# Performance work log

Hardware: AMD Instinct MI355X
Metric: run time of the kernel (lower is better)

## Reference

```python
import jax, jax.numpy as jnp
import numpy as np

HEAD_DIM = 128      # pooled entry dim (nope 64 + rope 64)
ROPE_DIM = 64       # trailing rotary slice
RATIO = 32          # compress_rate_csa: window stride; window width = 2*RATIO
ROPE_THETA = 10000.0
NEG = -1e9          # finite stand-in for -inf gate fill (softmax weight ~ 0)


def rotate_half_interleaved(x):
    # matches HF convention used with cos.repeat_interleave(2): pairs (x0,x1) -> (-x1,x0)
    x1 = x[..., 0::2]
    x2 = x[..., 1::2]
    return jnp.stack([-x2, x1], axis=-1).reshape(x.shape)


def setup_inputs() -> dict:
    key = jax.random.key(0)
    k1, k2, k3, k4 = jax.random.split(key, 4)
    B, S, H = 4, 8192, 4096
    return {
        "hidden_states": jax.random.normal(k1, (B, S, H), dtype=jnp.float32),
        "w_kv": jax.random.normal(k2, (H, 2 * HEAD_DIM), dtype=jnp.float32) * 0.02,
        "w_gate": jax.random.normal(k3, (H, 2 * HEAD_DIM), dtype=jnp.float32) * 0.02,
        "position_bias": jax.random.normal(k4, (2 * RATIO, HEAD_DIM), dtype=jnp.float32) * 0.02,
    }


def reference(hidden_states, w_kv, w_gate, position_bias):
    B, S, H = hidden_states.shape
    d, r = HEAD_DIM, RATIO
    n = S // r  # number of overlapping windows (stride r, width 2r)

    # projections C = H @ W^KV, Z = H @ W^Z   -> [B, S, 2d]
    kv = hidden_states @ w_kv
    gate = hidden_states @ w_gate

    chunk_kv = kv[:, : n * r].reshape(B, n, r, 2 * d)
    chunk_gate = gate[:, : n * r].reshape(B, n, r, 2 * d)

    # _overlap_pool: stitch each window's low-channel slice onto the prior
    # window's high-channel slice; window 0 prior half = 0 (kv) / -inf (gate).
    kv_lo, kv_hi = chunk_kv[..., :d], chunk_kv[..., d:]
    g_lo, g_hi = chunk_gate[..., :d], chunk_gate[..., d:]
    prev_kv = jnp.concatenate([jnp.zeros_like(kv_lo[:, :1]), kv_lo[:, :-1]], axis=1)
    prev_g = jnp.concatenate([jnp.full_like(g_lo[:, :1], NEG), g_lo[:, :-1]], axis=1)
    win_kv = jnp.concatenate([prev_kv, kv_hi], axis=2)   # [B, n, 2r, d]
    win_g = jnp.concatenate([prev_g, g_hi], axis=2)      # [B, n, 2r, d]

    # softmax-gated pooling over window tokens (per channel), with position bias
    w = jax.nn.softmax(win_g + position_bias[None, None], axis=2)
    pooled = jnp.sum(w * win_kv, axis=2)                 # [B, n, d]

    # RoPE on trailing rope slice at deterministic absolute window positions
    positions = jnp.arange(n, dtype=jnp.float32) * r     # first_pool_position = 0
    inv_freq = 1.0 / (ROPE_THETA ** (jnp.arange(0, ROPE_DIM, 2, dtype=jnp.float32) / ROPE_DIM))
    freqs = positions[:, None] * inv_freq[None, :]       # [n, ROPE_DIM/2]
    cos = jnp.repeat(jnp.cos(freqs), 2, axis=-1)         # [n, ROPE_DIM]
    sin = jnp.repeat(jnp.sin(freqs), 2, axis=-1)

    nope, rope = pooled[..., :-ROPE_DIM], pooled[..., -ROPE_DIM:]
    rotated = rope * cos[None] + rotate_half_interleaved(rope) * sin[None]
    return jnp.concatenate([nope, rotated], axis=-1)     # [B, n, d]
```

## Files before the change

### kernel.cpp

```cpp
#include <hip/hip_runtime.h>
#include <hip/hip_bf16.h>
#include <math.h>

typedef unsigned short ushort_t;
typedef __bf16 bf16x8 __attribute__((ext_vector_type(8)));
typedef float floatx4 __attribute__((ext_vector_type(4)));
typedef float floatx8 __attribute__((ext_vector_type(8)));

#define NEG_BIG -1000000000.0f

__device__ __forceinline__ float b2f(ushort_t u) {
  union { unsigned int i; float f; } v;
  v.i = ((unsigned int)u) << 16;
  return v.f;
}
__device__ __forceinline__ ushort_t f2b(float f) {
  union { float f; unsigned int i; } v;
  v.f = f;
  unsigned int r = v.i + 0x7fffu + ((v.i >> 16) & 1u);
  return (ushort_t)(r >> 16);
}

__device__ __forceinline__ float loadC(const float* p) { return *p; }
__device__ __forceinline__ float loadC(const ushort_t* p) { return b2f(*p); }
__device__ __forceinline__ void storeC(float* p, float v) { *p = v; }
__device__ __forceinline__ void storeC(ushort_t* p, float v) { *p = f2b(v); }

__global__ __launch_bounds__(256) void transpose_w_kernel(
    const float* __restrict__ w_kv, const float* __restrict__ w_gate,
    ushort_t* __restrict__ Wt) {
  __shared__ float tile[64][65];
  const int K0 = blockIdx.x * 64;
  const int N0c = blockIdx.y * 64;
  const float* src = (N0c < 256) ? w_kv : w_gate;
  const int N0 = N0c & 255;
  const int t = threadIdx.x;
#pragma unroll
  for (int i = 0; i < 16; ++i) {
    int l = t + 256 * i;
    int r = l >> 6, c = l & 63;
    tile[r][c] = src[(size_t)(K0 + r) * 256 + N0 + c];
  }
  __syncthreads();
#pragma unroll
  for (int i = 0; i < 16; ++i) {
    int l = t + 256 * i;
    int r = l >> 6, c = l & 63;
    Wt[(size_t)(N0c + r) * 4096 + K0 + c] = f2b(tile[c][r]);
  }
}

template <typename CT>
__global__ __launch_bounds__(256, 2) void gemm_kernel(
    const float* __restrict__ A,
    const ushort_t* __restrict__ Bt,
    CT* __restrict__ C) {
  constexpr int K = 4096;
  __shared__ __align__(16) ushort_t As[128 * 64];
  __shared__ __align__(16) ushort_t Bs[128 * 64];

  const int mt = blockIdx.x >> 2;
  const int nt = blockIdx.x & 3;
  const int m0 = mt * 128, n0 = nt * 128;
  const int tid = threadIdx.x;
  const int w = tid >> 6, lane = tid & 63;
  const int wm = w >> 1, wn = w & 1;
  const int sr = lane >> 3;
  const int sc = (lane & 7) * 8;
  const int ar = tid >> 3;
  const int ac = (tid & 7) * 8;
  const int q = lane >> 4, sid = lane & 15;

  floatx4 acc[4][4];
#pragma unroll
  for (int i = 0; i < 4; ++i)
#pragma unroll
    for (int j = 0; j < 4; ++j) acc[i][j] = (floatx4)0.0f;

  for (int kt = 0; kt < K; kt += 64) {
    __syncthreads();
#pragma unroll
    for (int i = 0; i < 4; ++i) {
      const int chunk = i * 4 + w;
      const int row = chunk * 8 + sr;
      const ushort_t* g = Bt + (size_t)(n0 + row) * K + kt + sc;
      __builtin_amdgcn_global_load_lds(
          (const __attribute__((address_space(1))) void*)g,
          (__attribute__((address_space(3))) void*)(Bs + chunk * 512), 16, 0, 0);
    }
#pragma unroll
    for (int p = 0; p < 4; ++p) {
      const int row = p * 32 + ar;
      const float* g = A + (size_t)(m0 + row) * K + kt + ac;
      floatx8 f = *(const floatx8*)g;
      bf16x8 h = __builtin_convertvector(f, bf16x8);
      *(bf16x8*)(As + row * 64 + ac) = h;
    }
    __syncthreads();

#pragma unroll
    for (int ks = 0; ks < 64; ks += 32) {
      bf16x8 af[4], bfr[4];
#pragma unroll
      for (int i = 0; i < 4; ++i)
        af[i] = *(const bf16x8*)(As + (wm * 64 + i * 16 + sid) * 64 + ks + q * 8);
#pragma unroll
      for (int j = 0; j < 4; ++j)
        bfr[j] = *(const bf16x8*)(Bs + (wn * 64 + j * 16 + sid) * 64 + ks + q * 8);
#pragma unroll
      for (int i = 0; i < 4; ++i)
#pragma unroll
        for (int j = 0; j < 4; ++j)
          acc[i][j] = __builtin_amdgcn_mfma_f32_16x16x32_bf16(af[i], bfr[j],
                                                              acc[i][j], 0, 0, 0);
    }
  }

#pragma unroll
  for (int i = 0; i < 4; ++i) {
#pragma unroll
    for (int j = 0; j < 4; ++j) {
#pragma unroll
      for (int r = 0; r < 4; ++r) {
        const int row = m0 + wm * 64 + i * 16 + q * 4 + r;
        const int col = n0 + wn * 64 + j * 16 + sid;
        storeC(&C[(size_t)row * 512 + col], acc[i][j][r]);
      }
    }
  }
}

template <typename CT>
__global__ __launch_bounds__(128) void pool_rope_kernel(
    const CT* __restrict__ C,
    const float* __restrict__ pb,
    float* __restrict__ out) {
  const int blk = blockIdx.x;
  const int j = blk & 255;
  const int d = threadIdx.x;

  const size_t base_hi = (size_t)blk * 32 * 512;
  const size_t base_lo = base_hi - (size_t)32 * 512;

  float m = -INFINITY, l = 0.f, o = 0.f;
#pragma unroll 8
  for (int t = 0; t < 64; ++t) {
    float g, kv;
    const float bias = pb[t * 128 + d];
    if (t < 32) {
      if (j == 0) {
        g = NEG_BIG;
        kv = 0.f;
      } else {
        g = loadC(&C[base_lo + (size_t)t * 512 + 256 + d]);
        kv = loadC(&C[base_lo + (size_t)t * 512 + d]);
      }
    } else {
      const int tt = t - 32;
      g = loadC(&C[base_hi + (size_t)tt * 512 + 384 + d]);
      kv = loadC(&C[base_hi + (size_t)tt * 512 + 128 + d]);
    }
    g += bias;
    const float mn = fmaxf(m, g);
    const float s = __expf(m - mn);
    const float p = __expf(g - mn);
    l = l * s + p;
    o = o * s + p * kv;
    m = mn;
  }
  const float pooled = o / l;

  float res;
  if (d < 64) {
    res = pooled;
  } else {
    const int rho = d - 64;
    const int i2 = rho >> 1;
    const float pos = (float)(j * 32);
    const float inv = powf(10000.0f, -(float)(2 * i2) / 64.0f);
    const float f = pos * inv;
    const float c = cosf(f), s2 = sinf(f);
    const float partner = __shfl_xor(pooled, 1, 64);
    res = (rho & 1) ? (pooled * c + partner * s2) : (pooled * c - partner * s2);
  }
  out[(size_t)blk * 128 + d] = res;
}

extern "C" void kernel_launch(void* const* d_in, const int* in_sizes, int n_in,
                              void* d_out, int out_size, void* d_ws,
                              size_t ws_size, hipStream_t stream) {
  (void)in_sizes; (void)n_in; (void)out_size;
  const float* hidden = (const float*)d_in[0];
  const float* w_kv = (const float*)d_in[1];
  const float* w_gate = (const float*)d_in[2];
  const float* pb = (const float*)d_in[3];
  float* out = (float*)d_out;

  ushort_t* Wt = (ushort_t*)d_ws;
  const size_t wt_bytes = (size_t)512 * 4096 * sizeof(ushort_t);
  char* cbase = (char*)d_ws + wt_bytes;
  const size_t c_elems = (size_t)32768 * 512;

  transpose_w_kernel<<<dim3(64, 8), 256, 0, stream>>>(w_kv, w_gate, Wt);

  if (ws_size >= wt_bytes + c_elems * sizeof(float)) {
    float* C = (float*)cbase;
    gemm_kernel<float><<<dim3(1024), 256, 0, stream>>>(hidden, Wt, C);
    pool_rope_kernel<float><<<dim3(1024), 128, 0, stream>>>(C, pb, out);
  } else {
    ushort_t* Cb = (ushort_t*)cbase;
    gemm_kernel<ushort_t><<<dim3(1024), 256, 0, stream>>>(hidden, Wt, Cb);
    pool_rope_kernel<ushort_t><<<dim3(1024), 128, 0, stream>>>(Cb, pb, out);
  }
}
```

Before: 939.6 us.

## Double-buffer GEMM tiles with XOR-swizzled LDS and split pooling across two halves

The GEMM now uses two LDS buffers so the next tile's global loads (B via direct-to-LDS, A via registers) overlap with MFMA on the current tile, needing one barrier per iteration. LDS rows are XOR-swizzled to cut bank conflicts on fragment reads, and block indices are remapped so concurrently running blocks share tiles. The pooling kernel splits each window's 64 tokens across two thread halves and merges the online-softmax states through shared memory. This doubles LDS use, which may lower occupancy.

```diff
diff --git a/kernel.cpp b/kernel.cpp
--- a/kernel.cpp
+++ b/kernel.cpp
@@ -56,20 +56,24 @@
     const ushort_t* __restrict__ Bt,
     CT* __restrict__ C) {
   constexpr int K = 4096;
-  __shared__ __align__(16) ushort_t As[128 * 64];
-  __shared__ __align__(16) ushort_t Bs[128 * 64];
-
-  const int mt = blockIdx.x >> 2;
-  const int nt = blockIdx.x & 3;
+  __shared__ __align__(16) ushort_t As[2][128 * 64];
+  __shared__ __align__(16) ushort_t Bs[2][128 * 64];
+
+  const int bid = blockIdx.x;
+  const int o = (bid & 7) * 128 + (bid >> 3);
+  const int mt = o >> 2;
+  const int nt = o & 3;
   const int m0 = mt * 128, n0 = nt * 128;
+
   const int tid = threadIdx.x;
   const int w = tid >> 6, lane = tid & 63;
   const int wm = w >> 1, wn = w & 1;
-  const int sr = lane >> 3;
-  const int sc = (lane & 7) * 8;
+  const int q = lane >> 4, sid = lane & 15;
+  const int bsr = lane >> 3;
+  const int bsc = ((lane & 7) ^ bsr) * 8;
   const int ar = tid >> 3;
-  const int ac = (tid & 7) * 8;
-  const int q = lane >> 4, sid = lane & 15;
+  const int aca = tid & 7;
+  const int acs = (aca ^ (ar & 7)) * 8;
 
   floatx4 acc[4][4];
 #pragma unroll
@@ -77,44 +81,82 @@
 #pragma unroll
     for (int j = 0; j < 4; ++j) acc[i][j] = (floatx4)0.0f;
 
-  for (int kt = 0; kt < K; kt += 64) {
+#define STAGE_B(BUF, KT)                                                      \
+  _Pragma("unroll")                                                           \
+  for (int i = 0; i < 4; ++i) {                                               \
+    const int chunk = i * 4 + w;                                              \
+    const int row = chunk * 8 + bsr;                                          \
+    const ushort_t* g = Bt + (size_t)(n0 + row) * K + (KT) + bsc;             \
+    __builtin_amdgcn_global_load_lds(                                         \
+        (const __attribute__((address_space(1))) void*)g,                     \
+        (__attribute__((address_space(3))) void*)(&Bs[BUF][chunk * 512]), 16, \
+        0, 0);                                                                \
+  }
+
+#define LOAD_A(KT, FREG)                                                      \
+  _Pragma("unroll")                                                           \
+  for (int p = 0; p < 4; ++p) {                                               \
+    const int row = p * 32 + ar;                                              \
+    FREG[p] = *(const floatx8*)(A + (size_t)(m0 + row) * K + (KT) + aca * 8); \
+  }
+
+#define WRITE_A(BUF, FREG)                                                    \
+  _Pragma("unroll")                                                           \
+  for (int p = 0; p < 4; ++p) {                                               \
+    const int row = p * 32 + ar;                                              \
+    *(bf16x8*)(&As[BUF][row * 64 + acs]) =                                    \
+        __builtin_convertvector(FREG[p], bf16x8);                             \
+  }
+
+#define COMPUTE_TILE(BUF)                                                     \
+  _Pragma("unroll")                                                           \
+  for (int ks = 0; ks < 64; ks += 32) {                                       \
+    const int kc = ks >> 3;                                       \
+    bf16x8 af[4], bfr[4];                                                     \
+    _Pragma("unroll")                                                         \
+    for (int i = 0; i < 4; ++i) {                                             \
+      const int ra = wm * 64 + i * 16 + sid;                                  \
+      af[i] =                                                                 \
+          *(const bf16x8*)(&As[BUF][ra * 64 + ((kc + q) ^ (sid & 7)) * 8]);   \
+    }                                                                         \
+    _Pragma("unroll")                                                         \
+    for (int j2 = 0; j2 < 4; ++j2) {                                          \
+      const int rb = wn * 64 + j2 * 16 + sid;                                 \
+      bfr[j2] =                                                               \
+          *(const bf16x8*)(&Bs[BUF][rb * 64 + ((kc + q) ^ (sid & 7)) * 8]);   \
+    }                                                                         \
+    _Pragma("unroll")                                                         \
+    for (int i = 0; i < 4; ++i)                                               \
+      _Pragma("unroll")                                                       \
+      for (int j2 = 0; j2 < 4; ++j2)                                          \
+        acc[i][j2] = __builtin_amdgcn_mfma_f32_16x16x32_bf16(                 \
+            af[i], bfr[j2], acc[i][j2], 0, 0, 0);                             \
+  }
+
+  {
+    STAGE_B(0, 0)
+    floatx8 f[4];
+    LOAD_A(0, f)
+    WRITE_A(0, f)
+  }
+  __syncthreads();
+
+  int cur = 0;
+  for (int kt = 64; kt < K; kt += 64) {
+    floatx8 f[4];
+    LOAD_A(kt, f)
+    STAGE_B(cur ^ 1, kt)
+    COMPUTE_TILE(cur)
+    WRITE_A(cur ^ 1, f)
     __syncthreads();
-#pragma unroll
-    for (int i = 0; i < 4; ++i) {
-      const int chunk = i * 4 + w;
-      const int row = chunk * 8 + sr;
-      const ushort_t* g = Bt + (size_t)(n0 + row) * K + kt + sc;
-      __builtin_amdgcn_global_load_lds(
-          (const __attribute__((address_space(1))) void*)g,
-          (__attribute__((address_space(3))) void*)(Bs + chunk * 512), 16, 0, 0);
-    }
-#pragma unroll
-    for (int p = 0; p < 4; ++p) {
-      const int row = p * 32 + ar;
-      const float* g = A + (size_t)(m0 + row) * K + kt + ac;
-      floatx8 f = *(const floatx8*)g;
-      bf16x8 h = __builtin_convertvector(f, bf16x8);
-      *(bf16x8*)(As + row * 64 + ac) = h;
-    }
-    __syncthreads();
-
-#pragma unroll
-    for (int ks = 0; ks < 64; ks += 32) {
-      bf16x8 af[4], bfr[4];
-#pragma unroll
-      for (int i = 0; i < 4; ++i)
-        af[i] = *(const bf16x8*)(As + (wm * 64 + i * 16 + sid) * 64 + ks + q * 8);
-#pragma unroll
-      for (int j = 0; j < 4; ++j)
-        bfr[j] = *(const bf16x8*)(Bs + (wn * 64 + j * 16 + sid) * 64 + ks + q * 8);
-#pragma unroll
-      for (int i = 0; i < 4; ++i)
-#pragma unroll
-        for (int j = 0; j < 4; ++j)
-          acc[i][j] = __builtin_amdgcn_mfma_f32_16x16x32_bf16(af[i], bfr[j],
-                                                              acc[i][j], 0, 0, 0);
-    }
-  }
+    cur ^= 1;
+  }
+  COMPUTE_TILE(cur)
+
+#undef STAGE_B
+#undef LOAD_A
+#undef WRITE_A
+#undef COMPUTE_TILE
 
 #pragma unroll
   for (int i = 0; i < 4; ++i) {
@@ -131,32 +173,34 @@
 }
 
 template <typename CT>
-__global__ __launch_bounds__(128) void pool_rope_kernel(
+__global__ __launch_bounds__(256) void pool_rope_kernel(
     const CT* __restrict__ C,
     const float* __restrict__ pb,
     float* __restrict__ out) {
   const int blk = blockIdx.x;
   const int j = blk & 255;
-  const int d = threadIdx.x;
+  const int tid = threadIdx.x;
+  const int d = tid & 127;
+  const int half = tid >> 7;
 
   const size_t base_hi = (size_t)blk * 32 * 512;
   const size_t base_lo = base_hi - (size_t)32 * 512;
 
   float m = -INFINITY, l = 0.f, o = 0.f;
+  const int tbase = half * 32;
 #pragma unroll 8
-  for (int t = 0; t < 64; ++t) {
+  for (int tt = 0; tt < 32; ++tt) {
     float g, kv;
-    const float bias = pb[t * 128 + d];
-    if (t < 32) {
+    const float bias = pb[(tbase + tt) * 128 + d];
+    if (half == 0) {
       if (j == 0) {
         g = NEG_BIG;
         kv = 0.f;
       } else {
-        g = loadC(&C[base_lo + (size_t)t * 512 + 256 + d]);
-        kv = loadC(&C[base_lo + (size_t)t * 512 + d]);
+        g = loadC(&C[base_lo + (size_t)tt * 512 + 256 + d]);
+        kv = loadC(&C[base_lo + (size_t)tt * 512 + d]);
       }
     } else {
-      const int tt = t - 32;
       g = loadC(&C[base_hi + (size_t)tt * 512 + 384 + d]);
       kv = loadC(&C[base_hi + (size_t)tt * 512 + 128 + d]);
     }
@@ -168,22 +212,37 @@
     o = o * s + p * kv;
     m = mn;
   }
-  const float pooled = o / l;
-
-  float res;
-  if (d < 64) {
-    res = pooled;
-  } else {
-    const int rho = d - 64;
-    const int i2 = rho >> 1;
-    const float pos = (float)(j * 32);
-    const float inv = powf(10000.0f, -(float)(2 * i2) / 64.0f);
-    const float f = pos * inv;
-    const float c = cosf(f), s2 = sinf(f);
-    const float partner = __shfl_xor(pooled, 1, 64);
-    res = (rho & 1) ? (pooled * c + partner * s2) : (pooled * c - partner * s2);
-  }
-  out[(size_t)blk * 128 + d] = res;
+
+  __shared__ float sm[128], sl[128], so[128];
+  if (half == 1) {
+    sm[d] = m;
+    sl[d] = l;
+    so[d] = o;
+  }
+  __syncthreads();
+  if (half == 0) {
+    const float m1 = sm[d], l1 = sl[d], o1 = so[d];
+    const float mn = fmaxf(m, m1);
+    const float s0 = __expf(m - mn), s1 = __expf(m1 - mn);
+    const float L = l * s0 + l1 * s1;
+    const float O = o * s0 + o1 * s1;
+    const float pooled = O / L;
+
+    float res;
+    if (d < 64) {
+      res = pooled;
+    } else {
+      const int rho = d - 64;
+      const int i2 = rho >> 1;
+      const float pos = (float)(j * 32);
+      const float inv = powf(10000.0f, -(float)(2 * i2) / 64.0f);
+      const float f = pos * inv;
+      const float c = cosf(f), s2 = sinf(f);
+      const float partner = __shfl_xor(pooled, 1, 64);
+      res = (rho & 1) ? (pooled * c + partner * s2) : (pooled * c - partner * s2);
+    }
+    out[(size_t)blk * 128 + d] = res;
+  }
 }
 
 extern "C" void kernel_launch(void* const* d_in, const int* in_sizes, int n_in,
@@ -204,12 +263,12 @@
   transpose_w_kernel<<<dim3(64, 8), 256, 0, stream>>>(w_kv, w_gate, Wt);
 
   if (ws_size >= wt_bytes + c_elems * sizeof(float)) {
-    float* C = (float*)cbase;
-    gemm_kernel<float><<<dim3(1024), 256, 0, stream>>>(hidden, Wt, C);
-    pool_rope_kernel<float><<<dim3(1024), 128, 0, stream>>>(C, pb, out);
+    float* Cf = (float*)cbase;
+    gemm_kernel<float><<<dim3(1024), 256, 0, stream>>>(hidden, Wt, Cf);
+    pool_rope_kernel<float><<<dim3(1024), 256, 0, stream>>>(Cf, pb, out);
   } else {
     ushort_t* Cb = (ushort_t*)cbase;
     gemm_kernel<ushort_t><<<dim3(1024), 256, 0, stream>>>(hidden, Wt, Cb);
-    pool_rope_kernel<ushort_t><<<dim3(1024), 128, 0, stream>>>(Cb, pb, out);
-  }
-}
+    pool_rope_kernel<ushort_t><<<dim3(1024), 256, 0, stream>>>(Cb, pb, out);
+  }
+}
```

Measured after the change: 931.6 us. No clear change (-0.9%).
